# Optimization experiments

Measured on AMD Instinct MI355X. Metric: run time of the kernel, lower is better.

Reference implementation:

```python
import jax, jax.numpy as jnp
import numpy as np

D_INNER = 256
D = 768
EPS = 1e-6


def _gelu(x):
    # torch nn.GELU() default is exact erf-based
    return jax.nn.gelu(x, approximate=False)


def setup_inputs() -> dict:
    key = jax.random.key(0)
    ks = jax.random.split(key, 16)
    N, M = 4096, 32768

    def xavier(k, shape):
        fan_in, fan_out = shape[0], shape[1]
        lim = np.sqrt(6.0 / (fan_in + fan_out))
        return jax.random.uniform(k, shape, jnp.float32, -lim, lim)

    return {
        "X": jax.random.normal(ks[0], (N, D), jnp.float32),
        "ctx_k": jax.random.normal(ks[1], (M, D_INNER), jnp.float32),
        "ctx_v": jax.random.normal(ks[2], (M, D), jnp.float32),
        "Wq_hop": xavier(ks[3], (D, D_INNER)),
        "alpha": jnp.zeros((), jnp.float32),
        "Wq_mol": xavier(ks[4], (D, D)),
        "Wk_mol": xavier(ks[5], (D, D)),
        "Wg": xavier(ks[6], (D, D)),
        "bg": jnp.zeros((D,), jnp.float32),
        "W1": xavier(ks[7], (D, 512)),
        "b1": jnp.zeros((512,), jnp.float32),
        "W2": xavier(ks[8], (512, 256)),
        "b2": jnp.zeros((256,), jnp.float32),
        "W3": xavier(ks[9], (256, 4)),
        "b3": jnp.zeros((4,), jnp.float32),
    }


def reference(X, ctx_k, ctx_v, Wq_hop, alpha, Wq_mol, Wk_mol, Wg, bg,
              W1, b1, W2, b2, W3, b3):
    # --- HopfieldContext: cross-attention to frozen context DB ---
    Q = X @ Wq_hop                                   # [N, 256]
    A_hop = jax.nn.softmax(Q @ ctx_k.T / np.sqrt(D_INNER), axis=-1)  # [N, M]
    enriched = A_hop @ ctx_v                          # [N, 768]
    blend = jax.nn.sigmoid(alpha)
    X2 = blend * enriched + (1.0 - blend) * X         # [N, 768]

    # --- MolAttention: dense self-attention adjacency ---
    Qm = X2 @ Wq_mol
    Km = X2 @ Wk_mol
    A = jax.nn.softmax(Qm @ Km.T / np.sqrt(D), axis=-1)  # [N, N]

    # --- degree-normalized aggregation + linear + GELU ---
    Dinv = 1.0 / jnp.clip(A.sum(-1, keepdims=True), 1e-8)  # [N, 1]
    Mfeat = _gelu(((A * Dinv) @ X2) @ Wg + bg)              # [N, 768]

    # --- NIGHead (eval mode: dropout = identity) ---
    h = X2 + Mfeat
    h = _gelu(h @ W1 + b1)
    h = _gelu(h @ W2 + b2)
    r = h @ W3 + b3                                   # [N, 4]
    mu = r[:, 0]
    v = jax.nn.softplus(r[:, 1]) + EPS
    a = jnp.minimum(jax.nn.softplus(r[:, 2]), 28.0) + 1.01
    b = jax.nn.softplus(r[:, 3]) + EPS
    return (mu, v, a, b)
```

## Files before the change

### kernel.cpp

```cpp
#include <hip/hip_runtime.h>
#include <hip/hip_bf16.h>
#include <math.h>

using bf16 = __hip_bfloat16;
typedef __attribute__((ext_vector_type(8))) short bf16x8;
typedef __attribute__((ext_vector_type(4))) float f32x4;

#define MFMA16(a, b, c) __builtin_amdgcn_mfma_f32_16x16x32_bf16((a), (b), (c), 0, 0, 0)
#define SMCAP 8.0f

__device__ __forceinline__ float gelu_exact(float x) {
    return 0.5f * x * (1.0f + erff(x * 0.70710678118654752f));
}
__device__ __forceinline__ float softplus_f(float x) {
    return x > 20.0f ? x : log1pf(__expf(x));
}
__device__ __forceinline__ float ldf(const void* p, size_t i, int f32) {
    return f32 ? ((const float*)p)[i] : __bfloat162float(((const bf16*)p)[i]);
}
__device__ __forceinline__ void stage16(const void* g, void* l) {
    __builtin_amdgcn_global_load_lds(
        (const __attribute__((address_space(1))) void*)g,
        (__attribute__((address_space(3))) void*)l, 16, 0, 0);
}

__global__ void sniff_k(const unsigned short* __restrict__ x, int* __restrict__ flag) {
    int t = threadIdx.x;
    unsigned short u = x[2 * t];
    bf16 h;
    __builtin_memcpy(&h, &u, 2);
    float f = __bfloat162float(h);
    int bad = !(fabsf(f) < 1000.0f);
    unsigned long long b = __ballot(bad);
    if (t == 0) flag[0] = (b != 0ULL) ? 1 : 0;
}

__global__ void cvt_k(const void* __restrict__ in, bf16* __restrict__ out,
                      size_t n, const int* __restrict__ flagp) {
    const int f32 = flagp[0];
    size_t i = (size_t)blockIdx.x * blockDim.x + threadIdx.x;
    if (i < n) out[i] = __float2bfloat16(ldf(in, i, f32));
}

__global__ void transpose_cvt(const void* __restrict__ in, bf16* __restrict__ out,
                              int R, int C, const int* __restrict__ flagp, int raw) {
    const int f32 = raw ? flagp[0] : 0;
    __shared__ bf16 tile[32][33];
    int bc = blockIdx.x * 32;
    int br = blockIdx.y * 32;
    int tx = threadIdx.x;
    int ty = threadIdx.y;
    for (int i = ty; i < 32; i += 8) {
        int r = br + i, c = bc + tx;
        tile[i][tx] = (r < R && c < C) ? __float2bfloat16(ldf(in, (size_t)r * C + c, f32))
                                       : __float2bfloat16(0.0f);
    }
    __syncthreads();
    for (int i = ty; i < 32; i += 8) {
        int r = br + tx, c = bc + i;
        if (r < R && c < C) out[(size_t)c * R + r] = tile[tx][i];
    }
}

__global__ void reshape_cm(const bf16* __restrict__ in, bf16* __restrict__ out, int M) {
    int idx = blockIdx.x * 256 + threadIdx.x;
    int m = idx / 768, e = idx % 768;
    out[(size_t)(e >> 8) * M * 256 + (size_t)m * 256 + (e & 255)] = in[idx];
}

__global__ void __launch_bounds__(256)
gemm_bt(const bf16* __restrict__ A, const bf16* __restrict__ Bt,
        bf16* __restrict__ C, const void* __restrict__ bias,
        const bf16* __restrict__ addend, int M, int N, int K, int act,
        const int* __restrict__ flagp) {
    const int f32 = flagp[0];
    const int tid = threadIdx.x;
    const int wave = tid >> 6;
    const int lane = tid & 63;
    const int l16 = lane & 15;
    const int lq = lane >> 4;
    const int m0 = blockIdx.y * 64 + wave * 16;
    const int n0 = blockIdx.x * 64;

    const bf16* arow = A + (size_t)(m0 + l16) * K + lq * 8;
    const bf16* brow = Bt + (size_t)(n0 + l16) * K + lq * 8;

    const f32x4 fz = {0.f, 0.f, 0.f, 0.f};
    f32x4 acc[4] = {fz, fz, fz, fz};

    for (int k = 0; k < K; k += 32) {
        bf16x8 af = *(const bf16x8*)(arow + k);
        #pragma unroll
        for (int ct = 0; ct < 4; ct++) {
            bf16x8 bfr = *(const bf16x8*)(brow + (size_t)ct * 16 * K + k);
            acc[ct] = MFMA16(af, bfr, acc[ct]);
        }
    }

    #pragma unroll
    for (int ct = 0; ct < 4; ct++) {
        int col = n0 + ct * 16 + l16;
        float bv = bias ? ldf(bias, col, f32) : 0.0f;
        #pragma unroll
        for (int r = 0; r < 4; r++) {
            int row = m0 + lq * 4 + r;
            float v = acc[ct][r] + bv;
            if (act == 1) v = gelu_exact(v);
            if (addend) v += __bfloat162float(addend[(size_t)row * N + col]);
            C[(size_t)row * N + col] = __float2bfloat16(v);
        }
    }
}

__global__ void __launch_bounds__(256)
flash3(const bf16* __restrict__ Q, const bf16* __restrict__ K,
       const bf16* __restrict__ VT, bf16* __restrict__ out,
       const bf16* __restrict__ Xres, const void* __restrict__ alpha_sc,
       int Mk, float scale, int mode, const int* __restrict__ flagp,
       int nsplit, float* __restrict__ Opart, float* __restrict__ lpart) {
    const int f32 = flagp[0];

    __shared__ __align__(16) char Qtile[32 * 1024];
    __shared__ __align__(16) bf16 Pbuf[64][72];
    __shared__ float lpw[4][64];

    const int tid = threadIdx.x;
    const int wave = tid >> 6;
    const int lane = tid & 63;
    const int l16 = lane & 15;
    const int lq = lane >> 4;

    const int m0 = blockIdx.y * 64;
    const int c0 = blockIdx.x * 192 + wave * 48;
    const int klen = Mk / nsplit;
    const int k0 = blockIdx.z * klen;

    #pragma unroll
    for (int kc = 0; kc < 8; kc++) {
        bf16x8 qv = *(const bf16x8*)(Q + (size_t)(m0 + wave * 16 + l16) * 256 + kc * 32 + lq * 8);
        *(bf16x8*)(Qtile + (wave * 8 + kc) * 1024 + lane * 16) = qv;
    }
    __syncthreads();

    const f32x4 fz = {0.f, 0.f, 0.f, 0.f};
    f32x4 acc[4][3];
    #pragma unroll
    for (int rt = 0; rt < 4; rt++)
        #pragma unroll
        for (int ct = 0; ct < 3; ct++) acc[rt][ct] = fz;
    float lsum[4][4];
    #pragma unroll
    for (int rt = 0; rt < 4; rt++)
        #pragma unroll
        for (int r = 0; r < 4; r++) lsum[rt][r] = 0.f;

    const bf16* kbase = K + (size_t)(wave * 16 + l16) * 256 + lq * 8;
    bf16x8 kcur[8], knext[8];
    #pragma unroll
    for (int j = 0; j < 8; j++)
        kcur[j] = *(const bf16x8*)(kbase + (size_t)k0 * 256 + j * 32);

    for (int kb = k0; kb < k0 + klen; kb += 64) {
        int kbn = (kb + 64 < k0 + klen) ? kb + 64 : kb;
        #pragma unroll
        for (int j = 0; j < 8; j++)
            knext[j] = *(const bf16x8*)(kbase + (size_t)kbn * 256 + j * 32);

        bf16x8 vb[3][2];
        #pragma unroll
        for (int ct = 0; ct < 3; ct++) {
            const bf16* vrow = VT + (size_t)(c0 + ct * 16 + l16) * Mk + kb + lq * 8;
            vb[ct][0] = *(const bf16x8*)(vrow);
            vb[ct][1] = *(const bf16x8*)(vrow + 32);
        }

        f32x4 s4[4] = {fz, fz, fz, fz};
        #pragma unroll
        for (int kc = 0; kc < 8; kc++) {
            #pragma unroll
            for (int rt = 0; rt < 4; rt++) {
                const bf16* qf = (const bf16*)(Qtile + ((rt * 8 + kc) << 10)) + lane * 8;
                s4[rt] = MFMA16(*(const bf16x8*)qf, kcur[kc], s4[rt]);
            }
        }

        #pragma unroll
        for (int rt = 0; rt < 4; rt++)
            #pragma unroll
            for (int r = 0; r < 4; r++) {
                float p = __expf(s4[rt][r] * scale - SMCAP);
                lsum[rt][r] += p;
                Pbuf[rt * 16 + lq * 4 + r][wave * 16 + l16] = __float2bfloat16(p);
            }
        __syncthreads();

        bf16x8 pa[4][2];
        #pragma unroll
        for (int rt = 0; rt < 4; rt++)
            #pragma unroll
            for (int kc2 = 0; kc2 < 2; kc2++)
                pa[rt][kc2] = *(const bf16x8*)&Pbuf[rt * 16 + l16][kc2 * 32 + lq * 8];
        #pragma unroll
        for (int ct = 0; ct < 3; ct++)
            #pragma unroll
            for (int rt = 0; rt < 4; rt++) {
                acc[rt][ct] = MFMA16(pa[rt][0], vb[ct][0], acc[rt][ct]);
                acc[rt][ct] = MFMA16(pa[rt][1], vb[ct][1], acc[rt][ct]);
            }
        __syncthreads();

        #pragma unroll
        for (int j = 0; j < 8; j++) kcur[j] = knext[j];
    }

    #pragma unroll
    for (int rt = 0; rt < 4; rt++)
        #pragma unroll
        for (int r = 0; r < 4; r++) {
            #pragma unroll
            for (int off = 1; off < 16; off <<= 1)
                lsum[rt][r] += __shfl_xor(lsum[rt][r], off, 64);
        }
    if (l16 == 0) {
        #pragma unroll
        for (int rt = 0; rt < 4; rt++)
            #pragma unroll
            for (int r = 0; r < 4; r++) lpw[wave][rt * 16 + lq * 4 + r] = lsum[rt][r];
    }
    __syncthreads();

    if (nsplit > 1) {
        if (blockIdx.x == 0 && wave == 0 && l16 == 0) {
            #pragma unroll
            for (int rt = 0; rt < 4; rt++)
                #pragma unroll
                for (int r = 0; r < 4; r++) {
                    int rw = rt * 16 + lq * 4 + r;
                    lpart[(size_t)blockIdx.z * 4096 + m0 + rw] =
                        lpw[0][rw] + lpw[1][rw] + lpw[2][rw] + lpw[3][rw];
                }
        }
        float* ob = Opart + (size_t)blockIdx.z * 4096 * 768;
        #pragma unroll
        for (int rt = 0; rt < 4; rt++)
            #pragma unroll
            for (int ct = 0; ct < 3; ct++) {
                int col = c0 + ct * 16 + l16;
                #pragma unroll
                for (int r = 0; r < 4; r++) {
                    int row = m0 + rt * 16 + lq * 4 + r;
                    ob[(size_t)row * 768 + col] = acc[rt][ct][r];
                }
            }
        return;
    }

    float blend = 1.0f, blend1 = 0.0f;
    if (mode == 1) {
        float av = ldf(alpha_sc, 0, f32);
        blend = 1.0f / (1.0f + __expf(-av));
        blend1 = 1.0f - blend;
    }
    #pragma unroll
    for (int rt = 0; rt < 4; rt++) {
        float li[4];
        #pragma unroll
        for (int r = 0; r < 4; r++) {
            int rw = rt * 16 + lq * 4 + r;
            li[r] = 1.0f / (lpw[0][rw] + lpw[1][rw] + lpw[2][rw] + lpw[3][rw]);
        }
        #pragma unroll
        for (int ct = 0; ct < 3; ct++) {
            int col = c0 + ct * 16 + l16;
            #pragma unroll
            for (int r = 0; r < 4; r++) {
                int row = m0 + rt * 16 + lq * 4 + r;
                float o = acc[rt][ct][r] * li[r];
                if (mode == 1)
                    o = blend * o + blend1 * __bfloat162float(Xres[(size_t)row * 768 + col]);
                out[(size_t)row * 768 + col] = __float2bfloat16(o);
            }
        }
    }
}

template <int CHUNKS>
__global__ void __launch_bounds__(256)
flash2(const bf16* __restrict__ Q, const bf16* __restrict__ Kc,
       const bf16* __restrict__ VT, bf16* __restrict__ out,
       const bf16* __restrict__ Xres, const void* __restrict__ alpha_sc,
       int Mk, float scale, int mode, const int* __restrict__ flagp,
       int nsplit, float* __restrict__ Opart, float* __restrict__ lpart) {
    const int f32 = flagp[0];
    constexpr int DK = CHUNKS * 256;

    __shared__ __align__(16) char Ktile[32 * 1024];
    __shared__ __align__(16) bf16 Pbuf[64][72];
    __shared__ float lL[64];

    const int tid = threadIdx.x;
    const int wave = tid >> 6;
    const int lane = tid & 63;
    const int l16 = lane & 15;
    const int lq = lane >> 4;

    const int m0 = blockIdx.y * 64;
    const int c0 = blockIdx.x * 192 + wave * 48;
    const int klen = Mk / nsplit;
    const int k0 = blockIdx.z * klen;

    const f32x4 fz = {0.f, 0.f, 0.f, 0.f};
    f32x4 acc[4][3];
    #pragma unroll
    for (int rt = 0; rt < 4; rt++)
        #pragma unroll
        for (int ct = 0; ct < 3; ct++) acc[rt][ct] = fz;

    float lrow[4] = {0.f, 0.f, 0.f, 0.f};

    const int qr = m0 + wave * 16 + l16;
    const size_t stage_lane_off = ((size_t)(wave * 16 + l16) * 256 + lq * 8) * 2;

    for (int kb = k0; kb < k0 + klen; kb += 64) {
        bf16x8 vb[3][2];
        #pragma unroll
        for (int ct = 0; ct < 3; ct++) {
            const bf16* vrow = VT + (size_t)(c0 + ct * 16 + l16) * Mk + kb + lq * 8;
            vb[ct][0] = *(const bf16x8*)(vrow);
            vb[ct][1] = *(const bf16x8*)(vrow + 32);
        }

        f32x4 s4[4] = {fz, fz, fz, fz};
        #pragma unroll
        for (int c = 0; c < CHUNKS; c++) {
            const char* gbase = (const char*)(Kc + (size_t)c * Mk * 256 + (size_t)kb * 256)
                                + stage_lane_off;
            #pragma unroll
            for (int j = 0; j < 8; j++)
                stage16(gbase + j * 64, Ktile + (wave * 8 + j) * 1024);
            __syncthreads();
            #pragma unroll
            for (int kc8 = 0; kc8 < 8; kc8++) {
                bf16x8 a = *(const bf16x8*)(Q + (size_t)qr * DK + c * 256 + kc8 * 32 + lq * 8);
                #pragma unroll
                for (int kt = 0; kt < 4; kt++) {
                    const bf16* kf = (const bf16*)(Ktile + ((kt * 8 + kc8) << 10)) + lane * 8;
                    s4[kt] = MFMA16(a, *(const bf16x8*)kf, s4[kt]);
                }
            }
            if (c != CHUNKS - 1) __syncthreads();
        }

        float ps[4] = {0.f, 0.f, 0.f, 0.f};
        #pragma unroll
        for (int kt = 0; kt < 4; kt++)
            #pragma unroll
            for (int r = 0; r < 4; r++) {
                float p = __expf(s4[kt][r] * scale - SMCAP);
                ps[r] += p;
                Pbuf[wave * 16 + lq * 4 + r][kt * 16 + l16] = __float2bfloat16(p);
            }
        #pragma unroll
        for (int off = 1; off < 16; off <<= 1)
            #pragma unroll
            for (int r = 0; r < 4; r++) ps[r] += __shfl_xor(ps[r], off, 64);
        #pragma unroll
        for (int r = 0; r < 4; r++) lrow[r] += ps[r];
        __syncthreads();

        bf16x8 pa[4][2];
        #pragma unroll
        for (int rt = 0; rt < 4; rt++)
            #pragma unroll
            for (int kc2 = 0; kc2 < 2; kc2++)
                pa[rt][kc2] = *(const bf16x8*)&Pbuf[rt * 16 + l16][kc2 * 32 + lq * 8];
        #pragma unroll
        for (int ct = 0; ct < 3; ct++)
            #pragma unroll
            for (int rt = 0; rt < 4; rt++) {
                acc[rt][ct] = MFMA16(pa[rt][0], vb[ct][0], acc[rt][ct]);
                acc[rt][ct] = MFMA16(pa[rt][1], vb[ct][1], acc[rt][ct]);
            }
    }

    if (nsplit > 1) {
        if (blockIdx.x == 0 && l16 == 0) {
            #pragma unroll
            for (int r = 0; r < 4; r++)
                lpart[(size_t)blockIdx.z * 4096 + m0 + wave * 16 + lq * 4 + r] = lrow[r];
        }
        float* ob = Opart + (size_t)blockIdx.z * 4096 * 768;
        #pragma unroll
        for (int rt = 0; rt < 4; rt++)
            #pragma unroll
            for (int ct = 0; ct < 3; ct++) {
                int col = c0 + ct * 16 + l16;
                #pragma unroll
                for (int r = 0; r < 4; r++) {
                    int row = m0 + rt * 16 + lq * 4 + r;
                    ob[(size_t)row * 768 + col] = acc[rt][ct][r];
                }
            }
        return;
    }

    __syncthreads();
    if (l16 == 0) {
        #pragma unroll
        for (int r = 0; r < 4; r++) lL[wave * 16 + lq * 4 + r] = lrow[r];
    }
    __syncthreads();

    float blend = 1.0f, blend1 = 0.0f;
    if (mode == 1) {
        float av = ldf(alpha_sc, 0, f32);
        blend = 1.0f / (1.0f + __expf(-av));
        blend1 = 1.0f - blend;
    }
    #pragma unroll
    for (int rt = 0; rt < 4; rt++) {
        float li[4];
        #pragma unroll
        for (int r = 0; r < 4; r++) li[r] = 1.0f / lL[rt * 16 + lq * 4 + r];
        #pragma unroll
        for (int ct = 0; ct < 3; ct++) {
            int col = c0 + ct * 16 + l16;
            #pragma unroll
            for (int r = 0; r < 4; r++) {
                int row = m0 + rt * 16 + lq * 4 + r;
                float o = acc[rt][ct][r] * li[r];
                if (mode == 1)
                    o = blend * o + blend1 * __bfloat162float(Xres[(size_t)row * 768 + col]);
                out[(size_t)row * 768 + col] = __float2bfloat16(o);
            }
        }
    }
}

__global__ void __launch_bounds__(256)
reduce3(const float* __restrict__ Opart, const float* __restrict__ lpart,
        bf16* __restrict__ out, const bf16* __restrict__ Xres,
        const void* __restrict__ alpha_sc, int nsplit, int mode,
        const int* __restrict__ flagp) {
    const int f32 = flagp[0];
    size_t idx = (size_t)blockIdx.x * 256 + threadIdx.x;
    int row = (int)(idx / 768);
    float L = 0.f, o = 0.f;
    for (int z = 0; z < nsplit; z++) {
        L += lpart[(size_t)z * 4096 + row];
        o += Opart[(size_t)z * 4096 * 768 + idx];
    }
    float val = o / L;
    if (mode == 1) {
        float av = ldf(alpha_sc, 0, f32);
        float blend = 1.0f / (1.0f + __expf(-av));
        val = blend * val + (1.0f - blend) * __bfloat162float(Xres[idx]);
    }
    out[idx] = __float2bfloat16(val);
}

__global__ void __launch_bounds__(256)
head_k(const bf16* __restrict__ h2, const void* __restrict__ W3,
       const void* __restrict__ b3, float* __restrict__ outp,
       const int* __restrict__ flagp) {
    const int f32 = flagp[0];
    int row = blockIdx.x * 4 + (threadIdx.x >> 6);
    int lane = threadIdx.x & 63;
    const bf16* hr = h2 + (size_t)row * 256 + lane * 4;
    float a0 = 0.f, a1 = 0.f, a2 = 0.f, a3 = 0.f;
    #pragma unroll
    for (int i = 0; i < 4; i++) {
        float hv = __bfloat162float(hr[i]);
        size_t wb = (size_t)(lane * 4 + i) * 4;
        a0 += hv * ldf(W3, wb + 0, f32);
        a1 += hv * ldf(W3, wb + 1, f32);
        a2 += hv * ldf(W3, wb + 2, f32);
        a3 += hv * ldf(W3, wb + 3, f32);
    }
    #pragma unroll
    for (int off = 1; off < 64; off <<= 1) {
        a0 += __shfl_xor(a0, off, 64);
        a1 += __shfl_xor(a1, off, 64);
        a2 += __shfl_xor(a2, off, 64);
        a3 += __shfl_xor(a3, off, 64);
    }
    if (lane == 0) {
        float r0 = a0 + ldf(b3, 0, f32);
        float r1 = a1 + ldf(b3, 1, f32);
        float r2 = a2 + ldf(b3, 2, f32);
        float r3 = a3 + ldf(b3, 3, f32);
        outp[row] = r0;
        outp[4096 + row] = softplus_f(r1) + 1e-6f;
        outp[8192 + row] = fminf(softplus_f(r2), 28.0f) + 1.01f;
        outp[12288 + row] = softplus_f(r3) + 1e-6f;
    }
}

extern "C" void kernel_launch(void* const* d_in, const int* in_sizes, int n_in,
                              void* d_out, int out_size, void* d_ws, size_t ws_size,
                              hipStream_t stream) {
    const void* X      = d_in[0];
    const void* ctx_k  = d_in[1];
    const void* ctx_v  = d_in[2];
    const void* Wq_hop = d_in[3];
    const void* alpha  = d_in[4];
    const void* Wq_mol = d_in[5];
    const void* Wk_mol = d_in[6];
    const void* Wg     = d_in[7];
    const void* bg     = d_in[8];
    const void* W1     = d_in[9];
    const void* b1     = d_in[10];
    const void* W2     = d_in[11];
    const void* b2     = d_in[12];
    const void* W3     = d_in[13];
    const void* b3     = d_in[14];
    float* out = (float*)d_out;

    char* wsb = (char*)d_ws;
    size_t off = 0;
    auto allocB = [&](size_t bytes) -> char* {
        char* p = wsb + off;
        off += (bytes + 255) & ~(size_t)255;
        return p;
    };
    int*  flag = (int*)allocB(256);
    bf16* Xbf  = (bf16*)allocB((size_t)4096 * 768 * 2);
    bf16* Kbf  = (bf16*)allocB((size_t)32768 * 256 * 2);
    bf16* WqhT = (bf16*)allocB((size_t)256 * 768 * 2);
    bf16* WqmT = (bf16*)allocB((size_t)768 * 768 * 2);
    bf16* WkmT = (bf16*)allocB((size_t)768 * 768 * 2);
    bf16* WgT  = (bf16*)allocB((size_t)768 * 768 * 2);
    bf16* W1T  = (bf16*)allocB((size_t)512 * 768 * 2);
    bf16* W2T  = (bf16*)allocB((size_t)256 * 512 * 2);
    bf16* Qb   = (bf16*)allocB((size_t)4096 * 256 * 2);
    bf16* X2   = (bf16*)allocB((size_t)4096 * 768 * 2);
    char* regA = allocB((size_t)768 * 32768 * 2);
    size_t needed_base = off;
    float* Opart = (float*)allocB((size_t)8 * 4096 * 768 * 4);
    float* lpart = (float*)allocB((size_t)8 * 4096 * 4);
    size_t needed_8 = off;
    size_t needed_4 = needed_base + ((size_t)4 * 4096 * 768 * 4 + (size_t)4 * 4096 * 4 + 512);
    if (ws_size < needed_base) return;
    const int nsplit = (ws_size >= needed_8) ? 8 : (ws_size >= needed_4 ? 4 : 1);

    bf16* VT = (bf16*)regA;
    size_t ra = 0;
    auto subA = [&](size_t bytes) -> bf16* {
        bf16* p = (bf16*)(regA + ra);
        ra += (bytes + 255) & ~(size_t)255;
        return p;
    };
    bf16* X2T = subA((size_t)768 * 4096 * 2);
    bf16* Qm  = subA((size_t)4096 * 768 * 2);
    bf16* Km  = subA((size_t)4096 * 768 * 2);
    bf16* Kmr = subA((size_t)4096 * 768 * 2);
    bf16* AX2 = subA((size_t)4096 * 768 * 2);
    bf16* hB  = subA((size_t)4096 * 768 * 2);
    bf16* h1B = subA((size_t)4096 * 512 * 2);
    bf16* h2B = subA((size_t)4096 * 256 * 2);

    sniff_k<<<1, 64, 0, stream>>>((const unsigned short*)X, flag);

    cvt_k<<<(4096 * 768) / 256, 256, 0, stream>>>(X, Xbf, (size_t)4096 * 768, flag);
    cvt_k<<<(32768 * 256) / 256, 256, 0, stream>>>(ctx_k, Kbf, (size_t)32768 * 256, flag);
    auto tr = [&](const void* in, bf16* o, int R, int C, int raw) {
        transpose_cvt<<<dim3(C / 32, R / 32), dim3(32, 8), 0, stream>>>(in, o, R, C, flag, raw);
    };
    tr(Wq_hop, WqhT, 768, 256, 1);
    tr(Wq_mol, WqmT, 768, 768, 1);
    tr(Wk_mol, WkmT, 768, 768, 1);
    tr(Wg, WgT, 768, 768, 1);
    tr(W1, W1T, 768, 512, 1);
    tr(W2, W2T, 512, 256, 1);
    tr(ctx_v, VT, 32768, 768, 1);

    gemm_bt<<<dim3(4, 64), 256, 0, stream>>>(
        Xbf, WqhT, Qb, nullptr, nullptr, 4096, 256, 768, 0, flag);

    flash3<<<dim3(4, 64, nsplit), 256, 0, stream>>>(
        Qb, Kbf, VT, X2, Xbf, alpha, 32768, 0.0625f, 1, flag,
        nsplit, Opart, lpart);
    if (nsplit > 1)
        reduce3<<<(4096 * 768) / 256, 256, 0, stream>>>(
            Opart, lpart, X2, Xbf, alpha, nsplit, 1, flag);

    tr(X2, X2T, 4096, 768, 0);

    gemm_bt<<<dim3(12, 64), 256, 0, stream>>>(
        X2, WqmT, Qm, nullptr, nullptr, 4096, 768, 768, 0, flag);
    gemm_bt<<<dim3(12, 64), 256, 0, stream>>>(
        X2, WkmT, Km, nullptr, nullptr, 4096, 768, 768, 0, flag);
    reshape_cm<<<(4096 * 768) / 256, 256, 0, stream>>>(Km, Kmr, 4096);

    flash2<3><<<dim3(4, 64, nsplit), 256, 0, stream>>>(
        Qm, Kmr, X2T, AX2, Xbf, alpha, 4096, 0.036084391824351615f, 0, flag,
        nsplit, Opart, lpart);
    if (nsplit > 1)
        reduce3<<<(4096 * 768) / 256, 256, 0, stream>>>(
            Opart, lpart, AX2, Xbf, alpha, nsplit, 0, flag);

    gemm_bt<<<dim3(12, 64), 256, 0, stream>>>(
        AX2, WgT, hB, bg, X2, 4096, 768, 768, 1, flag);

    gemm_bt<<<dim3(8, 64), 256, 0, stream>>>(
        hB, W1T, h1B, b1, nullptr, 4096, 512, 768, 1, flag);
    gemm_bt<<<dim3(4, 64), 256, 0, stream>>>(
        h1B, W2T, h2B, b2, nullptr, 4096, 256, 512, 1, flag);

    head_k<<<1024, 256, 0, stream>>>(h2B, W3, b3, out, flag);
}
```

Baseline: 1.845 ms.

## Restructure Hopfield attention kernel to 128-row tiles with LDS-staged K and register Q

The cross-attention kernel now processes 128 query rows per block instead of 64, halving the grid in y. Q fragments stay in registers, and K tiles are staged into LDS with async global-to-LDS loads prefetched one step ahead. Each V load is reused across twice as many rows, which cuts V traffic from global memory. In exchange, register pressure rises (a 128x48 accumulator per wave), the P buffer grows, fewer blocks are launched, and the launch-bounds hint asks for two blocks per CU.

```diff
diff --git a/kernel.cpp b/kernel.cpp
--- a/kernel.cpp
+++ b/kernel.cpp
@@ -112,17 +112,17 @@
     }
 }
 
-__global__ void __launch_bounds__(256)
-flash3(const bf16* __restrict__ Q, const bf16* __restrict__ K,
+__global__ void __launch_bounds__(256, 2)
+flash5(const bf16* __restrict__ Q, const bf16* __restrict__ K,
        const bf16* __restrict__ VT, bf16* __restrict__ out,
        const bf16* __restrict__ Xres, const void* __restrict__ alpha_sc,
        int Mk, float scale, int mode, const int* __restrict__ flagp,
        int nsplit, float* __restrict__ Opart, float* __restrict__ lpart) {
     const int f32 = flagp[0];
 
-    __shared__ __align__(16) char Qtile[32 * 1024];
-    __shared__ __align__(16) bf16 Pbuf[64][72];
-    __shared__ float lpw[4][64];
+    __shared__ __align__(16) char Ktile[32 * 1024];
+    __shared__ __align__(16) bf16 Pbuf[128][136];
+    __shared__ float lL[128];
 
     const int tid = threadIdx.x;
     const int wave = tid >> 6;
@@ -130,119 +130,108 @@
     const int l16 = lane & 15;
     const int lq = lane >> 4;
 
-    const int m0 = blockIdx.y * 64;
+    const int m0 = blockIdx.y * 128;
     const int c0 = blockIdx.x * 192 + wave * 48;
     const int klen = Mk / nsplit;
     const int k0 = blockIdx.z * klen;
-
-    #pragma unroll
-    for (int kc = 0; kc < 8; kc++) {
-        bf16x8 qv = *(const bf16x8*)(Q + (size_t)(m0 + wave * 16 + l16) * 256 + kc * 32 + lq * 8);
-        *(bf16x8*)(Qtile + (wave * 8 + kc) * 1024 + lane * 16) = qv;
-    }
-    __syncthreads();
+    const int kend = k0 + klen;
+
+    bf16x8 qf[2][8];
+    #pragma unroll
+    for (int rt = 0; rt < 2; rt++)
+        #pragma unroll
+        for (int kc = 0; kc < 8; kc++)
+            qf[rt][kc] = *(const bf16x8*)(Q + (size_t)(m0 + wave * 32 + rt * 16 + l16) * 256 +
+                                          kc * 32 + lq * 8);
 
     const f32x4 fz = {0.f, 0.f, 0.f, 0.f};
-    f32x4 acc[4][3];
-    #pragma unroll
-    for (int rt = 0; rt < 4; rt++)
+    f32x4 acc[8][3];
+    #pragma unroll
+    for (int rt = 0; rt < 8; rt++)
         #pragma unroll
         for (int ct = 0; ct < 3; ct++) acc[rt][ct] = fz;
-    float lsum[4][4];
-    #pragma unroll
-    for (int rt = 0; rt < 4; rt++)
+    float lsum[2][4];
+    #pragma unroll
+    for (int rt = 0; rt < 2; rt++)
         #pragma unroll
         for (int r = 0; r < 4; r++) lsum[rt][r] = 0.f;
 
-    const bf16* kbase = K + (size_t)(wave * 16 + l16) * 256 + lq * 8;
-    bf16x8 kcur[8], knext[8];
-    #pragma unroll
-    for (int j = 0; j < 8; j++)
-        kcur[j] = *(const bf16x8*)(kbase + (size_t)k0 * 256 + j * 32);
-
-    for (int kb = k0; kb < k0 + klen; kb += 64) {
-        int kbn = (kb + 64 < k0 + klen) ? kb + 64 : kb;
-        #pragma unroll
-        for (int j = 0; j < 8; j++)
-            knext[j] = *(const bf16x8*)(kbase + (size_t)kbn * 256 + j * 32);
-
-        bf16x8 vb[3][2];
-        #pragma unroll
-        for (int ct = 0; ct < 3; ct++) {
-            const bf16* vrow = VT + (size_t)(c0 + ct * 16 + l16) * Mk + kb + lq * 8;
-            vb[ct][0] = *(const bf16x8*)(vrow);
-            vb[ct][1] = *(const bf16x8*)(vrow + 32);
-        }
-
-        f32x4 s4[4] = {fz, fz, fz, fz};
+    const size_t kgoff = ((size_t)(wave * 16 + l16) * 256 + lq * 8) * 2;
+    auto stageK = [&](int kb) {
+        const char* g = (const char*)K + (size_t)kb * 512 + kgoff;
+        #pragma unroll
+        for (int kc = 0; kc < 8; kc++)
+            stage16(g + kc * 64, Ktile + (wave * 8 + kc) * 1024);
+    };
+    stageK(k0);
+
+    for (int kb = k0; kb < kend; kb += 64) {
+        __syncthreads();
+
+        f32x4 s4[2][4] = {{fz, fz, fz, fz}, {fz, fz, fz, fz}};
         #pragma unroll
         for (int kc = 0; kc < 8; kc++) {
             #pragma unroll
-            for (int rt = 0; rt < 4; rt++) {
-                const bf16* qf = (const bf16*)(Qtile + ((rt * 8 + kc) << 10)) + lane * 8;
-                s4[rt] = MFMA16(*(const bf16x8*)qf, kcur[kc], s4[rt]);
-            }
-        }
-
-        #pragma unroll
-        for (int rt = 0; rt < 4; rt++)
-            #pragma unroll
-            for (int r = 0; r < 4; r++) {
-                float p = __expf(s4[rt][r] * scale - SMCAP);
-                lsum[rt][r] += p;
-                Pbuf[rt * 16 + lq * 4 + r][wave * 16 + l16] = __float2bfloat16(p);
-            }
+            for (int kt = 0; kt < 4; kt++) {
+                bf16x8 kf = *(const bf16x8*)(Ktile + ((kt * 8 + kc) << 10) + (size_t)lane * 16);
+                s4[0][kt] = MFMA16(qf[0][kc], kf, s4[0][kt]);
+                s4[1][kt] = MFMA16(qf[1][kc], kf, s4[1][kt]);
+            }
+        }
+        #pragma unroll
+        for (int rt = 0; rt < 2; rt++)
+            #pragma unroll
+            for (int kt = 0; kt < 4; kt++)
+                #pragma unroll
+                for (int r = 0; r < 4; r++) {
+                    float p = __expf(s4[rt][kt][r] * scale - SMCAP);
+                    lsum[rt][r] += p;
+                    Pbuf[wave * 32 + rt * 16 + lq * 4 + r][kt * 16 + l16] = __float2bfloat16(p);
+                }
         __syncthreads();
 
-        bf16x8 pa[4][2];
-        #pragma unroll
-        for (int rt = 0; rt < 4; rt++)
-            #pragma unroll
-            for (int kc2 = 0; kc2 < 2; kc2++)
-                pa[rt][kc2] = *(const bf16x8*)&Pbuf[rt * 16 + l16][kc2 * 32 + lq * 8];
-        #pragma unroll
-        for (int ct = 0; ct < 3; ct++)
-            #pragma unroll
-            for (int rt = 0; rt < 4; rt++) {
-                acc[rt][ct] = MFMA16(pa[rt][0], vb[ct][0], acc[rt][ct]);
-                acc[rt][ct] = MFMA16(pa[rt][1], vb[ct][1], acc[rt][ct]);
-            }
-        __syncthreads();
-
-        #pragma unroll
-        for (int j = 0; j < 8; j++) kcur[j] = knext[j];
-    }
-
-    #pragma unroll
-    for (int rt = 0; rt < 4; rt++)
+        if (kb + 64 < kend) stageK(kb + 64);
+
+        #pragma unroll
+        for (int kc2 = 0; kc2 < 2; kc2++) {
+            bf16x8 vb0, vb1, vb2;
+            {
+                const bf16* v0 = VT + (size_t)(c0 + l16) * Mk + kb + kc2 * 32 + lq * 8;
+                vb0 = *(const bf16x8*)(v0);
+                vb1 = *(const bf16x8*)(v0 + (size_t)16 * Mk);
+                vb2 = *(const bf16x8*)(v0 + (size_t)32 * Mk);
+            }
+            #pragma unroll
+            for (int rt = 0; rt < 8; rt++) {
+                bf16x8 pa = *(const bf16x8*)&Pbuf[rt * 16 + l16][kc2 * 32 + lq * 8];
+                acc[rt][0] = MFMA16(pa, vb0, acc[rt][0]);
+                acc[rt][1] = MFMA16(pa, vb1, acc[rt][1]);
+                acc[rt][2] = MFMA16(pa, vb2, acc[rt][2]);
+            }
+        }
+    }
+
+    #pragma unroll
+    for (int rt = 0; rt < 2; rt++)
         #pragma unroll
         for (int r = 0; r < 4; r++) {
             #pragma unroll
             for (int off = 1; off < 16; off <<= 1)
                 lsum[rt][r] += __shfl_xor(lsum[rt][r], off, 64);
         }
-    if (l16 == 0) {
-        #pragma unroll
-        for (int rt = 0; rt < 4; rt++)
-            #pragma unroll
-            for (int r = 0; r < 4; r++) lpw[wave][rt * 16 + lq * 4 + r] = lsum[rt][r];
-    }
-    __syncthreads();
 
     if (nsplit > 1) {
-        if (blockIdx.x == 0 && wave == 0 && l16 == 0) {
-            #pragma unroll
-            for (int rt = 0; rt < 4; rt++)
+        if (blockIdx.x == 0 && l16 == 0) {
+            #pragma unroll
+            for (int rt = 0; rt < 2; rt++)
                 #pragma unroll
-                for (int r = 0; r < 4; r++) {
-                    int rw = rt * 16 + lq * 4 + r;
-                    lpart[(size_t)blockIdx.z * 4096 + m0 + rw] =
-                        lpw[0][rw] + lpw[1][rw] + lpw[2][rw] + lpw[3][rw];
-                }
+                for (int r = 0; r < 4; r++)
+                    lpart[(size_t)blockIdx.z * 4096 + m0 + wave * 32 + rt * 16 + lq * 4 + r] =
+                        lsum[rt][r];
         }
         float* ob = Opart + (size_t)blockIdx.z * 4096 * 768;
         #pragma unroll
-        for (int rt = 0; rt < 4; rt++)
+        for (int rt = 0; rt < 8; rt++)
             #pragma unroll
             for (int ct = 0; ct < 3; ct++) {
                 int col = c0 + ct * 16 + l16;
@@ -255,6 +244,16 @@
         return;
     }
 
+    __syncthreads();
+    if (l16 == 0) {
+        #pragma unroll
+        for (int rt = 0; rt < 2; rt++)
+            #pragma unroll
+            for (int r = 0; r < 4; r++)
+                lL[wave * 32 + rt * 16 + lq * 4 + r] = lsum[rt][r];
+    }
+    __syncthreads();
+
     float blend = 1.0f, blend1 = 0.0f;
     if (mode == 1) {
         float av = ldf(alpha_sc, 0, f32);
@@ -262,20 +261,14 @@
         blend1 = 1.0f - blend;
     }
     #pragma unroll
-    for (int rt = 0; rt < 4; rt++) {
-        float li[4];
-        #pragma unroll
-        for (int r = 0; r < 4; r++) {
-            int rw = rt * 16 + lq * 4 + r;
-            li[r] = 1.0f / (lpw[0][rw] + lpw[1][rw] + lpw[2][rw] + lpw[3][rw]);
-        }
+    for (int rt = 0; rt < 8; rt++) {
         #pragma unroll
         for (int ct = 0; ct < 3; ct++) {
             int col = c0 + ct * 16 + l16;
             #pragma unroll
             for (int r = 0; r < 4; r++) {
                 int row = m0 + rt * 16 + lq * 4 + r;
-                float o = acc[rt][ct][r] * li[r];
+                float o = acc[rt][ct][r] / lL[rt * 16 + lq * 4 + r];
                 if (mode == 1)
                     o = blend * o + blend1 * __bfloat162float(Xres[(size_t)row * 768 + col]);
                 out[(size_t)row * 768 + col] = __float2bfloat16(o);
@@ -577,7 +570,7 @@
     gemm_bt<<<dim3(4, 64), 256, 0, stream>>>(
         Xbf, WqhT, Qb, nullptr, nullptr, 4096, 256, 768, 0, flag);
 
-    flash3<<<dim3(4, 64, nsplit), 256, 0, stream>>>(
+    flash5<<<dim3(4, 32, nsplit), 256, 0, stream>>>(
         Qb, Kbf, VT, X2, Xbf, alpha, 32768, 0.0625f, 1, flag,
         nsplit, Opart, lpart);
     if (nsplit > 1)
```

After: 1.629 ms. 1.13x faster.
